# Optimization experiments

Measured on AMD Instinct MI355X. Metric: run time of the kernel, lower is better.

Reference implementation:

```python
import jax, jax.numpy as jnp
import numpy as np

N_P, N_V, N_C, N_A = 8000, 3000, 1500, 6000
CLS = N_C
D = 128
E = 150000
N_TOT = N_P + N_V + N_C + N_A
LAMBDA1 = 1.0


def _cal_matrix(A):
    # row-normalize, leaving all-zero rows untouched (matches cal_matrix)
    d = jnp.sum(A, axis=1)
    safe = jnp.where(d > 0, d, 1.0)
    return jnp.where((d > 0)[:, None], A / safe[:, None], A)


def _linear(x, W, b):
    return x @ W.T + b


def _gru(x, h, Wih, Whh, bih, bhh):
    # torch.nn.GRUCell semantics; gate order r, z, n
    gi = x @ Wih.T + bih
    gh = h @ Whh.T + bhh
    ir, iz, inn = jnp.split(gi, 3, axis=1)
    hr, hz, hn = jnp.split(gh, 3, axis=1)
    r = jax.nn.sigmoid(ir + hr)
    z = jax.nn.sigmoid(iz + hz)
    n = jnp.tanh(inn + r * hn)
    return (1.0 - z) * n + z * h


def _ce_soft(pred, label):
    # torch CrossEntropyLoss with probabilistic targets; NOTE: pred is already
    # softmaxed in the original, so log_softmax is applied on top (faithful double softmax)
    return -jnp.mean(jnp.sum(label * jax.nn.log_softmax(pred, axis=1), axis=1))


def _fuse(e0, e1, W2, b2, W3, b3):
    # attention fusion: leaky_relu(., 0) == relu; softmax over the NODE axis (faithful)
    a = jnp.concatenate([_linear(e0, W2, b2), _linear(e1, W3, b3)], axis=0)  # [2N,1]
    alpha = jax.nn.softmax(jax.nn.relu(a).reshape(2, -1, 1), axis=1)
    return jax.nn.relu(jnp.sum(alpha * jnp.stack([e0, e1], axis=0), axis=0))


def _forward(feat_P, feat_V, feat_C, feat_A, W1, b1, W2, b2, W3, b3,
             L00W, L00b, L01W, L01b, L10W, L10b, L11W, L11b, L12W, L12b,
             g0_Wih, g0_Whh, g0_bih, g0_bhh, g1_Wih, g1_Whh, g1_bih, g1_bhh,
             rel_emb, adj00, adj01, adj10, adj11, adj12, clsA, clsP, clsV, u_s, u_d):
    # self embeddings via shared linear1
    self_P = _linear(feat_P, W1, b1)
    self_V = _linear(feat_V, W1, b1)
    self_C = _linear(feat_C, W1, b1)
    self_A = _linear(feat_A, W1, b1)
    loss_tcp = jnp.float32(0.0)
    # ---- meta-path 0: V -> P -> A (GRUCell 0) ----
    pred = jax.nn.softmax(_linear(feat_V, L00W, L00b), axis=1)        # [N_V, CLS]
    loss_tcp += _ce_soft(pred, clsV)
    tcp = jnp.sum(pred * clsV, axis=1, keepdims=True)                 # bmm([N,1,C],[N,C,1])
    h = adj00 @ (tcp * feat_V)                                        # [N_P, D]
    state_P0 = _gru(feat_P, h, g0_Wih, g0_Whh, g0_bih, g0_bhh)
    pred = jax.nn.softmax(_linear(state_P0, L01W, L01b), axis=1)
    loss_tcp += _ce_soft(pred, clsP)
    tcp = jnp.sum(pred * clsP, axis=1, keepdims=True)
    h = adj01 @ (tcp * state_P0)                                      # [N_A, D]
    state_A0 = _gru(feat_A, h, g0_Wih, g0_Whh, g0_bih, g0_bhh)
    # ---- meta-path 1: A -> P -> V -> C (GRUCell 1) ----
    pred = jax.nn.softmax(_linear(feat_A, L10W, L10b), axis=1)
    loss_tcp += _ce_soft(pred, clsA)
    tcp = jnp.sum(pred * clsA, axis=1, keepdims=True)
    h = adj10 @ (tcp * feat_A)                                        # [N_P, D]
    state_P1 = _gru(feat_P, h, g1_Wih, g1_Whh, g1_bih, g1_bhh)        # appended 3rd, unused by fusion
    pred = jax.nn.softmax(_linear(state_P1, L11W, L11b), axis=1)
    loss_tcp += _ce_soft(pred, clsP)
    tcp = jnp.sum(pred * clsP, axis=1, keepdims=True)
    h = adj11 @ (tcp * state_P1)                                      # [N_V, D]
    state_V1 = _gru(feat_V, h, g1_Wih, g1_Whh, g1_bih, g1_bhh)
    pred = jax.nn.softmax(_linear(state_V1, L12W, L12b), axis=1)
    loss_tcp += _ce_soft(pred, clsV)
    tcp = jnp.sum(pred * clsV, axis=1, keepdims=True)
    h = adj12 @ (tcp * state_V1)                                      # [N_C, D]
    state_C1 = _gru(feat_C, h, g1_Wih, g1_Whh, g1_bih, g1_bhh)
    # ---- attention fusion of (self_emb, first GRU state) per node type ----
    emb_P = _fuse(self_P, state_P0, W2, b2, W3, b3)
    emb_V = _fuse(self_V, state_V1, W2, b2, W3, b3)
    emb_C = _fuse(self_C, state_C1, W2, b2, W3, b3)
    emb_A = _fuse(self_A, state_A0, W2, b2, W3, b3)
    final_ent = jnp.concatenate([emb_P, emb_V, emb_C, emb_A], axis=0)  # order P,V,C,A
    # ---- link scoring ----
    lab_d = u_d[:, 2].astype(jnp.float32)
    lab_s = u_s[:, 2].astype(jnp.float32)
    M_r = rel_emb[u_d[:, 3]]
    inner_d = jnp.sum(M_r * jnp.tanh(final_ent[u_d[:, 0]] + final_ent[u_d[:, 1]]), axis=1)
    inner_s = jnp.sum(final_ent[u_s[:, 0]] * final_ent[u_s[:, 1]], axis=1)
    base = -jnp.sum(jax.nn.log_sigmoid(lab_d * inner_d)) - jnp.sum(jax.nn.log_sigmoid(lab_s * inner_s))
    # l2_loss_emb is 0 in the original; l2_loss is computed but never added to loss_emb
    loss = base + LAMBDA1 * loss_tcp
    return loss, final_ent, rel_emb


def setup_inputs():
    key = jax.random.key(0)
    ki = iter(jax.random.split(key, 48))
    def nk():
        return next(ki)
    def xav(o, i):  # xavier_normal_
        return jax.random.normal(nk(), (o, i), jnp.float32) * jnp.sqrt(2.0 / (o + i))
    def uni(shape):  # torch GRUCell default init
        k = 1.0 / float(np.sqrt(D))
        return jax.random.uniform(nk(), shape, jnp.float32, -k, k)
    def radj(o, i, p=0.003):  # raw binary adjacency
        return (jax.random.uniform(nk(), (o, i)) < p).astype(jnp.float32)

    feat_P = jax.random.normal(nk(), (N_P, D), jnp.float32)
    feat_V = jax.random.normal(nk(), (N_V, D), jnp.float32)
    feat_C = jax.random.normal(nk(), (N_C, D), jnp.float32)
    feat_A = jax.random.normal(nk(), (N_A, D), jnp.float32)
    A00 = radj(N_P, N_V); A01 = radj(N_A, N_P)
    A10 = radj(N_P, N_A); A11 = radj(N_V, N_P); A12 = radj(N_C, N_V)

    inp = dict(
        feat_P=feat_P, feat_V=feat_V, feat_C=feat_C, feat_A=feat_A,
        W1=xav(D, D), b1=jnp.zeros((D,), jnp.float32),
        W2=xav(1, D), b2=jnp.zeros((1,), jnp.float32),
        W3=xav(1, D), b3=jnp.zeros((1,), jnp.float32),
        L00W=xav(CLS, D), L00b=jnp.zeros((CLS,), jnp.float32),
        L01W=xav(CLS, D), L01b=jnp.zeros((CLS,), jnp.float32),
        L10W=xav(CLS, D), L10b=jnp.zeros((CLS,), jnp.float32),
        L11W=xav(CLS, D), L11b=jnp.zeros((CLS,), jnp.float32),
        L12W=xav(CLS, D), L12b=jnp.zeros((CLS,), jnp.float32),
        g0_Wih=uni((3 * D, D)), g0_Whh=uni((3 * D, D)), g0_bih=uni((3 * D,)), g0_bhh=uni((3 * D,)),
        g1_Wih=uni((3 * D, D)), g1_Whh=uni((3 * D, D)), g1_bih=uni((3 * D,)), g1_bhh=uni((3 * D,)),
        rel_emb=jax.random.normal(nk(), (12, D), jnp.float32),
        adj00=_cal_matrix(A00), adj01=_cal_matrix(A01),
        adj10=_cal_matrix(A10), adj11=_cal_matrix(A11), adj12=_cal_matrix(A12),
        clsA=_cal_matrix((A12 @ (A11 @ A10)).T),   # [N_A, CLS]
        clsP=_cal_matrix((A12 @ A11).T),           # [N_P, CLS]
        clsV=_cal_matrix(A12.T),                   # [N_V, CLS]
    )

    def edges(n_cols):
        i = jax.random.randint(nk(), (E,), 0, N_TOT)
        j = jax.random.randint(nk(), (E,), 0, N_TOT)
        lab = jax.random.randint(nk(), (E,), 0, 2) * 2 - 1  # labels in {-1,+1}
        cols = [i, j, lab]
        if n_cols == 4:
            cols.append(jax.random.randint(nk(), (E,), 0, 12))
        return jnp.stack(cols, axis=1)

    inp['u_s'] = edges(3)
    inp['u_d'] = edges(4)
    return inp


def reference(feat_P, feat_V, feat_C, feat_A, W1, b1, W2, b2, W3, b3,
              L00W, L00b, L01W, L01b, L10W, L10b, L11W, L11b, L12W, L12b,
              g0_Wih, g0_Whh, g0_bih, g0_bhh, g1_Wih, g1_Whh, g1_bih, g1_bhh,
              rel_emb, adj00, adj01, adj10, adj11, adj12, clsA, clsP, clsV, u_s, u_d):
    return _forward(feat_P, feat_V, feat_C, feat_A, W1, b1, W2, b2, W3, b3,
                    L00W, L00b, L01W, L01b, L10W, L10b, L11W, L11b, L12W, L12b,
                    g0_Wih, g0_Whh, g0_bih, g0_bhh, g1_Wih, g1_Whh, g1_bih, g1_bhh,
                    rel_emb, adj00, adj01, adj10, adj11, adj12, clsA, clsP, clsV, u_s, u_d)
```

## Files before the change

### kernel.cpp

```cpp
#include <hip/hip_runtime.h>
#include <cstdint>
#include <cstddef>

#define DEV_INLINE __device__ __forceinline__

typedef __attribute__((ext_vector_type(8))) short bf16x8;
typedef __attribute__((ext_vector_type(16))) float f32x16;
struct __align__(8) US4 { unsigned short u[4]; };

DEV_INLINE unsigned short f2bf(float x) {
  unsigned u = __float_as_uint(x);
  return (unsigned short)((u + 0x7FFFu + ((u >> 16) & 1u)) >> 16);
}
DEV_INLINE float2 bfpair(unsigned v) {
  return make_float2(__uint_as_float(v << 16), __uint_as_float(v & 0xFFFF0000u));
}

struct CvtSeg { const float* src; unsigned short* dst; int n; int nblk; };
struct CvtArgs { CvtSeg seg[16]; int nseg; };

__global__ __launch_bounds__(256) void convert_bf16_many(CvtArgs args) {
  int b = blockIdx.x;
  int s = 0;
  while (s < args.nseg && b >= args.seg[s].nblk) { b -= args.seg[s].nblk; ++s; }
  if (s >= args.nseg) return;
  int base = b * 1024 + threadIdx.x * 4;
  if (base >= args.seg[s].n) return;
  float4 v = *reinterpret_cast<const float4*>(args.seg[s].src + base);
  US4 o;
  o.u[0] = f2bf(v.x); o.u[1] = f2bf(v.y); o.u[2] = f2bf(v.z); o.u[3] = f2bf(v.w);
  *reinterpret_cast<US4*>(args.seg[s].dst + base) = o;
}

DEV_INLINE void gemm_stage(const unsigned short* __restrict__ Xb,
                           const unsigned short* __restrict__ Wb,
                           int N, int O, int bm, int bn,
                           unsigned short* Xs, unsigned short* Ws)
{
  const int tid = threadIdx.x;
#pragma unroll
  for (int i = 0; i < 8; ++i) {
    int s = tid + 256 * i;
    int row = s >> 4, c16 = s & 15;
    uint4 v = make_uint4(0, 0, 0, 0);
    int gr = bm + row;
    if (gr < N) v = *reinterpret_cast<const uint4*>(Xb + (size_t)gr * 128 + c16 * 8);
    *reinterpret_cast<uint4*>(&Xs[(row * 16 + (c16 ^ (row & 7))) * 8]) = v;
  }
#pragma unroll
  for (int i = 0; i < 4; ++i) {
    int s = tid + 256 * i;
    int row = s >> 4, c16 = s & 15;
    uint4 v = make_uint4(0, 0, 0, 0);
    int gw = bn + row;
    if (gw < O) v = *reinterpret_cast<const uint4*>(Wb + (size_t)gw * 128 + c16 * 8);
    *reinterpret_cast<uint4*>(&Ws[(row * 16 + (c16 ^ (row & 7))) * 8]) = v;
  }
  __syncthreads();
}

DEV_INLINE void gemm_mfma(const unsigned short* Xs, const unsigned short* Ws,
                          f32x16& acc0, f32x16& acc1)
{
  const int tid = threadIdx.x;
  const int wave = tid >> 6, lane = tid & 63;
  const int l31 = lane & 31, lhi = lane >> 5;
#pragma unroll
  for (int i = 0; i < 16; ++i) { acc0[i] = 0.f; acc1[i] = 0.f; }
  const int ar = wave * 32 + l31;
#pragma unroll
  for (int ks = 0; ks < 8; ++ks) {
    int c16 = ks * 2 + lhi;
    bf16x8 a  = *reinterpret_cast<const bf16x8*>(&Xs[(ar * 16 + (c16 ^ (ar & 7))) * 8]);
    bf16x8 b0 = *reinterpret_cast<const bf16x8*>(&Ws[(l31 * 16 + (c16 ^ (l31 & 7))) * 8]);
    int br1 = 32 + l31;
    bf16x8 b1 = *reinterpret_cast<const bf16x8*>(&Ws[(br1 * 16 + (c16 ^ (br1 & 7))) * 8]);
    acc0 = __builtin_amdgcn_mfma_f32_32x32x16_bf16(a, b0, acc0, 0, 0, 0);
    acc1 = __builtin_amdgcn_mfma_f32_32x32x16_bf16(a, b1, acc1, 0, 0, 0);
  }
}

DEV_INLINE void gemm_body(
    const unsigned short* __restrict__ Xb, const unsigned short* __restrict__ Wb,
    const float* __restrict__ bias, float* __restrict__ C, int N, int O,
    int bm, int bn, unsigned short* Xs, unsigned short* Ws)
{
  gemm_stage(Xb, Wb, N, O, bm, bn, Xs, Ws);
  const int tid = threadIdx.x;
  const int wave = tid >> 6, lane = tid & 63;
  const int l31 = lane & 31, lhi = lane >> 5;
  f32x16 acc0, acc1;
  gemm_mfma(Xs, Ws, acc0, acc1);
#pragma unroll
  for (int reg = 0; reg < 16; ++reg) {
    int r = bm + wave * 32 + (reg & 3) + 8 * (reg >> 2) + 4 * lhi;
    if (r < N) {
      int c0 = bn + l31;
      if (c0 < O) C[(size_t)r * O + c0] = acc0[reg] + bias[c0];
      int c1 = bn + 32 + l31;
      if (c1 < O) C[(size_t)r * O + c1] = acc1[reg] + bias[c1];
    }
  }
}

DEV_INLINE void gemm_body_b(
    const unsigned short* __restrict__ Xb, const unsigned short* __restrict__ Wb,
    const float* __restrict__ bias, unsigned short* __restrict__ Cb, int N, int O,
    int bm, int bn, unsigned short* Xs, unsigned short* Ws)
{
  gemm_stage(Xb, Wb, N, O, bm, bn, Xs, Ws);
  const int tid = threadIdx.x;
  const int wave = tid >> 6, lane = tid & 63;
  const int l31 = lane & 31, lhi = lane >> 5;
  f32x16 acc0, acc1;
  gemm_mfma(Xs, Ws, acc0, acc1);
#pragma unroll
  for (int reg = 0; reg < 16; ++reg) {
    int r = bm + wave * 32 + (reg & 3) + 8 * (reg >> 2) + 4 * lhi;
    if (r < N) {
      int c0 = bn + l31;
      if (c0 < O) Cb[(size_t)r * O + c0] = f2bf(acc0[reg] + bias[c0]);
      int c1 = bn + 32 + l31;
      if (c1 < O) Cb[(size_t)r * O + c1] = f2bf(acc1[reg] + bias[c1]);
    }
  }
}

struct GSeg { const unsigned short* X; const unsigned short* W; const float* bias;
              float* C; int N; int O; int blk0; int xblk; };
struct GSegs { GSeg s[8]; int nseg; };

__global__ __launch_bounds__(256) void gemm_bf16_gseg(GSegs gs) {
  __shared__ __align__(16) unsigned short Xs[128 * 128];
  __shared__ __align__(16) unsigned short Ws[64 * 128];
  int bx = blockIdx.x;
  int si = 0;
  while (si + 1 < gs.nseg && bx >= gs.s[si + 1].blk0) ++si;
  const GSeg& g = gs.s[si];
  int b = bx - g.blk0;
  gemm_body(g.X, g.W, g.bias, g.C, g.N, g.O, (b % g.xblk) * 128, (b / g.xblk) * 64, Xs, Ws);
}

struct GBSeg { const unsigned short* X; const unsigned short* W; const float* bias;
               unsigned short* C; int N; int O; int blk0; int xblk; };
struct GBSegs { GBSeg s[4]; int nseg; };

__global__ __launch_bounds__(256) void gemm_bf16o_gseg(GBSegs gs) {
  __shared__ __align__(16) unsigned short Xs[128 * 128];
  __shared__ __align__(16) unsigned short Ws[64 * 128];
  int bx = blockIdx.x;
  int si = 0;
  while (si + 1 < gs.nseg && bx >= gs.s[si + 1].blk0) ++si;
  const GBSeg& g = gs.s[si];
  int b = bx - g.blk0;
  gemm_body_b(g.X, g.W, g.bias, g.C, g.N, g.O, (b % g.xblk) * 128, (b / g.xblk) * 64, Xs, Ws);
}

DEV_INLINE void spmv_body(const float* __restrict__ A, const float* __restrict__ Xs,
                          float* __restrict__ H, unsigned short* __restrict__ Hb,
                          int row, int K, float (*red)[128])
{
  int tid = threadIdx.x, wave = tid >> 6, lane = tid & 63;
  const float4* Arow = reinterpret_cast<const float4*>(A + (size_t)row * K);
  int K4 = K >> 2;
  float acc0 = 0.f, acc1 = 0.f;
  int base = wave * 64;
  int q = base + lane;
  float4 a = (base < K4 && q < K4) ? Arow[q] : make_float4(0.f, 0.f, 0.f, 0.f);
  for (; base < K4; base += 256) {
    int nb = base + 256;
    int nq = nb + lane;
    float4 an = (nb < K4 && nq < K4) ? Arow[nq] : make_float4(0.f, 0.f, 0.f, 0.f);
#pragma unroll
    for (int c = 0; c < 4; ++c) {
      float av = (c == 0) ? a.x : (c == 1) ? a.y : (c == 2) ? a.z : a.w;
      unsigned long long mm = __ballot(av != 0.f);
      while (mm) {
        int b = __builtin_ctzll(mm);
        mm &= mm - 1;
        float v = __shfl(av, b);
        int jj = (base + b) * 4 + c;
        const float* xr = Xs + (size_t)jj * 128;
        acc0 += v * xr[lane];
        acc1 += v * xr[lane + 64];
      }
    }
    a = an;
  }
  red[wave][lane] = acc0;
  red[wave][lane + 64] = acc1;
  __syncthreads();
  if (wave == 0) {
    float r0 = red[0][lane] + red[1][lane] + red[2][lane] + red[3][lane];
    float r1 = red[0][lane + 64] + red[1][lane + 64] + red[2][lane + 64] + red[3][lane + 64];
    H[(size_t)row * 128 + lane] = r0;
    H[(size_t)row * 128 + 64 + lane] = r1;
    Hb[(size_t)row * 128 + lane] = f2bf(r0);
    Hb[(size_t)row * 128 + 64 + lane] = f2bf(r1);
  }
}

__global__ __launch_bounds__(256) void spmv_scan(
    const float* __restrict__ A, const float* __restrict__ Xs,
    float* __restrict__ H, unsigned short* __restrict__ Hb, int M, int K)
{
  __shared__ float red[4][128];
  spmv_body(A, Xs, H, Hb, blockIdx.x, K, red);
}

__global__ __launch_bounds__(256) void spmv_scan2(
    const float* __restrict__ A0, const float* __restrict__ X0,
    float* __restrict__ H0, unsigned short* __restrict__ H0b, int M0, int K0,
    const float* __restrict__ A1, const float* __restrict__ X1,
    float* __restrict__ H1, unsigned short* __restrict__ H1b, int K1)
{
  __shared__ float red[4][128];
  if ((int)blockIdx.x < M0) spmv_body(A0, X0, H0, H0b, blockIdx.x, K0, red);
  else                      spmv_body(A1, X1, H1, H1b, blockIdx.x - M0, K1, red);
}

DEV_INLINE void ghgru_body(
    const unsigned short* __restrict__ Hb, const unsigned short* __restrict__ Whhb,
    const float* __restrict__ bhh, const float* __restrict__ gi,
    const float* __restrict__ hv, float* __restrict__ out,
    unsigned short* __restrict__ outb, int M, int bm, unsigned short* As)
{
  const int tid = threadIdx.x;
#pragma unroll
  for (int i = 0; i < 2; ++i) {
    int s = tid + 256 * i;
    int row = s >> 4, c16 = s & 15;
    uint4 v = make_uint4(0, 0, 0, 0);
    int gr = bm + row;
    if (gr < M) v = *reinterpret_cast<const uint4*>(Hb + (size_t)gr * 128 + c16 * 8);
    *reinterpret_cast<uint4*>(&As[(row * 16 + (c16 ^ (row & 7))) * 8]) = v;
  }
  __syncthreads();

  const int wave = tid >> 6, lane = tid & 63;
  const int l31 = lane & 31, lhi = lane >> 5;
  const int d = wave * 32 + l31;

  f32x16 ar, az, an;
#pragma unroll
  for (int i = 0; i < 16; ++i) { ar[i] = 0.f; az[i] = 0.f; an[i] = 0.f; }

#pragma unroll
  for (int ks = 0; ks < 8; ++ks) {
    int c16 = ks * 2 + lhi;
    bf16x8 a = *reinterpret_cast<const bf16x8*>(&As[(l31 * 16 + (c16 ^ (l31 & 7))) * 8]);
    const unsigned short* wb = Whhb + (size_t)c16 * 8;
    bf16x8 br = *reinterpret_cast<const bf16x8*>(wb + (size_t)d * 128);
    bf16x8 bz = *reinterpret_cast<const bf16x8*>(wb + (size_t)(128 + d) * 128);
    bf16x8 bn = *reinterpret_cast<const bf16x8*>(wb + (size_t)(256 + d) * 128);
    ar = __builtin_amdgcn_mfma_f32_32x32x16_bf16(a, br, ar, 0, 0, 0);
    az = __builtin_amdgcn_mfma_f32_32x32x16_bf16(a, bz, az, 0, 0, 0);
    an = __builtin_amdgcn_mfma_f32_32x32x16_bf16(a, bn, an, 0, 0, 0);
  }

  const float b_r = bhh[d], b_z = bhh[128 + d], b_n = bhh[256 + d];
#pragma unroll
  for (int reg = 0; reg < 16; ++reg) {
    int r = bm + (reg & 3) + 8 * (reg >> 2) + 4 * lhi;
    if (r < M) {
      const float* gir = gi + (size_t)r * 384;
      float rr = 1.f / (1.f + __expf(-(gir[d] + ar[reg] + b_r)));
      float zz = 1.f / (1.f + __expf(-(gir[128 + d] + az[reg] + b_z)));
      float nn = tanhf(gir[256 + d] + rr * (an[reg] + b_n));
      float h = hv[(size_t)r * 128 + d];
      float o = (1.f - zz) * nn + zz * h;
      out[(size_t)r * 128 + d] = o;
      outb[(size_t)r * 128 + d] = f2bf(o);
    }
  }
}

__global__ __launch_bounds__(256) void gh_gru(
    const unsigned short* __restrict__ Hb, const unsigned short* __restrict__ Whhb,
    const float* __restrict__ bhh, const float* __restrict__ gi,
    const float* __restrict__ hv, float* __restrict__ out,
    unsigned short* __restrict__ outb, int M)
{
  __shared__ __align__(16) unsigned short As[32 * 128];
  ghgru_body(Hb, Whhb, bhh, gi, hv, out, outb, M, blockIdx.x * 32, As);
}

__global__ __launch_bounds__(256) void gh_gru2(
    const unsigned short* Hb0, const unsigned short* Whh0, const float* bhh0,
    const float* gi0, const float* hv0, float* out0, unsigned short* outb0,
    int M0, int nblk0,
    const unsigned short* Hb1, const unsigned short* Whh1, const float* bhh1,
    const float* gi1, const float* hv1, float* out1, unsigned short* outb1, int M1)
{
  __shared__ __align__(16) unsigned short As[32 * 128];
  if ((int)blockIdx.x < nblk0)
    ghgru_body(Hb0, Whh0, bhh0, gi0, hv0, out0, outb0, M0, blockIdx.x * 32, As);
  else
    ghgru_body(Hb1, Whh1, bhh1, gi1, hv1, out1, outb1, M1, (blockIdx.x - nblk0) * 32, As);
}

DEV_INLINE void rowops_body(int lane, const float4* __restrict__ lr,
                            const float4* __restrict__ cr,
                            const float* __restrict__ srcrow,
                            float* __restrict__ scaledrow, float* __restrict__ cep)
{
  float4 e[6];
  float m = -3.4e38f;
#pragma unroll
  for (int k = 0; k < 6; ++k) {
    int idx = k * 64 + lane;
    if (idx < 375) {
      e[k] = lr[idx];
      m = fmaxf(m, fmaxf(fmaxf(e[k].x, e[k].y), fmaxf(e[k].z, e[k].w)));
    } else {
      e[k] = make_float4(-3.4e38f, -3.4e38f, -3.4e38f, -3.4e38f);
    }
  }
#pragma unroll
  for (int o = 1; o < 64; o <<= 1) m = fmaxf(m, __shfl_xor(m, o));
  float z = 0.f;
#pragma unroll
  for (int k = 0; k < 6; ++k) {
    e[k].x = __expf(e[k].x - m); e[k].y = __expf(e[k].y - m);
    e[k].z = __expf(e[k].z - m); e[k].w = __expf(e[k].w - m);
    z += (e[k].x + e[k].y) + (e[k].z + e[k].w);
  }
#pragma unroll
  for (int o = 1; o < 64; o <<= 1) z += __shfl_xor(z, o);
  float invZ1 = 1.0f / z;
  float m2 = invZ1;
  float t = 0.f, ls = 0.f, z2 = 0.f;
#pragma unroll
  for (int k = 0; k < 6; ++k) {
    int idx = k * 64 + lane;
    if (idx < 375) {
      float4 c = cr[idx];
      float px = e[k].x * invZ1, py = e[k].y * invZ1;
      float pz = e[k].z * invZ1, pw = e[k].w * invZ1;
      t  += c.x * px + c.y * py + c.z * pz + c.w * pw;
      ls += (c.x + c.y) + (c.z + c.w);
      z2 += __expf(px - m2) + __expf(py - m2) + __expf(pz - m2) + __expf(pw - m2);
    }
  }
#pragma unroll
  for (int o = 1; o < 64; o <<= 1) {
    t += __shfl_xor(t, o); ls += __shfl_xor(ls, o); z2 += __shfl_xor(z2, o);
  }
  if (lane == 0) *cep = t - ls * (m2 + logf(z2));
  scaledrow[lane]      = t * srcrow[lane];
  scaledrow[lane + 64] = t * srcrow[lane + 64];
}

__global__ __launch_bounds__(256) void rowops2(
    const float* lgA, const float* clsA_, const float* srcA, float* scA, float* ceA, int nA,
    const float* lgB, const float* clsB_, const float* srcB, float* scB, float* ceB, int nB)
{
  int gw = (blockIdx.x * 256 + threadIdx.x) >> 6;
  if (gw >= nA + nB) return;
  int lane = threadIdx.x & 63;
  if (gw < nA) {
    rowops_body(lane,
                reinterpret_cast<const float4*>(lgA + (size_t)gw * 1500),
                reinterpret_cast<const float4*>(clsA_ + (size_t)gw * 1500),
                srcA + (size_t)gw * 128, scA + (size_t)gw * 128, ceA + gw);
  } else {
    int r = gw - nA;
    rowops_body(lane,
                reinterpret_cast<const float4*>(lgB + (size_t)r * 1500),
                reinterpret_cast<const float4*>(clsB_ + (size_t)r * 1500),
                srcB + (size_t)r * 128, scB + (size_t)r * 128, ceB + r);
  }
}

DEV_INLINE void rowops_body_b(int lane, const unsigned* __restrict__ lrb,
                              const float2* __restrict__ cr2,
                              const float* __restrict__ srcrow,
                              float* __restrict__ scaledrow, float* __restrict__ cep)
{
  float2 e[12];
  float m = -3.4e38f;
#pragma unroll
  for (int k = 0; k < 12; ++k) {
    int idx = k * 64 + lane;
    if (idx < 750) {
      e[k] = bfpair(lrb[idx]);
      m = fmaxf(m, fmaxf(e[k].x, e[k].y));
    } else {
      e[k] = make_float2(-3.4e38f, -3.4e38f);
    }
  }
#pragma unroll
  for (int o = 1; o < 64; o <<= 1) m = fmaxf(m, __shfl_xor(m, o));
  float z = 0.f;
#pragma unroll
  for (int k = 0; k < 12; ++k) {
    e[k].x = __expf(e[k].x - m); e[k].y = __expf(e[k].y - m);
    z += e[k].x + e[k].y;
  }
#pragma unroll
  for (int o = 1; o < 64; o <<= 1) z += __shfl_xor(z, o);
  float invZ1 = 1.0f / z;
  float m2 = invZ1;
  float t = 0.f, ls = 0.f, z2 = 0.f;
#pragma unroll
  for (int k = 0; k < 12; ++k) {
    int idx = k * 64 + lane;
    if (idx < 750) {
      float2 c = cr2[idx];
      float px = e[k].x * invZ1, py = e[k].y * invZ1;
      t  += c.x * px + c.y * py;
      ls += c.x + c.y;
      z2 += __expf(px - m2) + __expf(py - m2);
    }
  }
#pragma unroll
  for (int o = 1; o < 64; o <<= 1) {
    t += __shfl_xor(t, o); ls += __shfl_xor(ls, o); z2 += __shfl_xor(z2, o);
  }
  if (lane == 0) *cep = t - ls * (m2 + logf(z2));
  scaledrow[lane]      = t * srcrow[lane];
  scaledrow[lane + 64] = t * srcrow[lane + 64];
}

__global__ __launch_bounds__(256) void rowops2b(
    const unsigned* lgA, const float* clsA_, const float* srcA, float* scA, float* ceA, int nA,
    const unsigned* lgB, const float* clsB_, const float* srcB, float* scB, float* ceB, int nB)
{
  int gw = (blockIdx.x * 256 + threadIdx.x) >> 6;
  if (gw >= nA + nB) return;
  int lane = threadIdx.x & 63;
  if (gw < nA) {
    rowops_body_b(lane, lgA + (size_t)gw * 750,
                  reinterpret_cast<const float2*>(clsA_ + (size_t)gw * 1500),
                  srcA + (size_t)gw * 128, scA + (size_t)gw * 128, ceA + gw);
  } else {
    int r = gw - nA;
    rowops_body_b(lane, lgB + (size_t)r * 750,
                  reinterpret_cast<const float2*>(clsB_ + (size_t)r * 1500),
                  srcB + (size_t)r * 128, scB + (size_t)r * 128, ceB + r);
  }
}

__global__ __launch_bounds__(256) void rowops1b(
    const unsigned* lg, const float* cls, const float* src, float* sc, float* ce, int n)
{
  int gw = (blockIdx.x * 256 + threadIdx.x) >> 6;
  if (gw >= n) return;
  int lane = threadIdx.x & 63;
  rowops_body_b(lane, lg + (size_t)gw * 750,
                reinterpret_cast<const float2*>(cls + (size_t)gw * 1500),
                src + (size_t)gw * 128, sc + (size_t)gw * 128, ce + gw);
}

__global__ __launch_bounds__(256) void fuse_scores_all(
    const float* __restrict__ e0, const float* __restrict__ e1,
    const float* __restrict__ W2, const float* __restrict__ b2,
    const float* __restrict__ W3, const float* __restrict__ b3,
    float* __restrict__ s0, float* __restrict__ s1)
{
  int lane = threadIdx.x & 63;
  int row = (blockIdx.x * 256 + threadIdx.x) >> 6;
  if (row >= 18500) return;
  float a0 = e0[(size_t)row * 128 + lane] * W2[lane] + e0[(size_t)row * 128 + 64 + lane] * W2[64 + lane];
  float a1 = e1[(size_t)row * 128 + lane] * W3[lane] + e1[(size_t)row * 128 + 64 + lane] * W3[64 + lane];
#pragma unroll
  for (int o = 32; o > 0; o >>= 1) { a0 += __shfl_down(a0, o); a1 += __shfl_down(a1, o); }
  if (lane == 0) {
    s0[row] = fmaxf(a0 + b2[0], 0.f);
    s1[row] = fmaxf(a1 + b3[0], 0.f);
  }
}

__global__ __launch_bounds__(1024) void denom4(
    const float* __restrict__ s0, const float* __restrict__ s1,
    float* __restrict__ den)
{
  __shared__ float red[1024];
  const int ns[4]   = {8000, 3000, 1500, 6000};
  const int offs[4] = {0, 8000, 11000, 12500};
  int b = blockIdx.x;
  int n = ns[b];
  const float* p0 = s0 + offs[b];
  const float* p1 = s1 + offs[b];
  int tid = threadIdx.x;
  float m = -3.4e38f;
  for (int i = tid; i < n; i += 1024) m = fmaxf(m, p0[i]);
  red[tid] = m; __syncthreads();
  for (int s = 512; s > 0; s >>= 1) { if (tid < s) red[tid] = fmaxf(red[tid], red[tid + s]); __syncthreads(); }
  float m0 = red[0]; __syncthreads();
  float z = 0.f;
  for (int i = tid; i < n; i += 1024) z += __expf(p0[i] - m0);
  red[tid] = z; __syncthreads();
  for (int s = 512; s > 0; s >>= 1) { if (tid < s) red[tid] += red[tid + s]; __syncthreads(); }
  float Z0 = red[0]; __syncthreads();
  m = -3.4e38f;
  for (int i = tid; i < n; i += 1024) m = fmaxf(m, p1[i]);
  red[tid] = m; __syncthreads();
  for (int s = 512; s > 0; s >>= 1) { if (tid < s) red[tid] = fmaxf(red[tid], red[tid + s]); __syncthreads(); }
  float m1 = red[0]; __syncthreads();
  z = 0.f;
  for (int i = tid; i < n; i += 1024) z += __expf(p1[i] - m1);
  red[tid] = z; __syncthreads();
  for (int s = 512; s > 0; s >>= 1) { if (tid < s) red[tid] += red[tid + s]; __syncthreads(); }
  if (tid == 0) { den[b * 4] = m0; den[b * 4 + 1] = Z0; den[b * 4 + 2] = m1; den[b * 4 + 3] = red[0]; }
}

__global__ __launch_bounds__(256) void fuse_emb_all(
    const float* __restrict__ e0, const float* __restrict__ e1,
    const float* __restrict__ s0, const float* __restrict__ s1,
    const float* __restrict__ den, const float* __restrict__ rel,
    float* __restrict__ fe, unsigned short* __restrict__ feb,
    float* __restrict__ rel_out, unsigned* __restrict__ ctr)
{
  int t = blockIdx.x * 256 + threadIdx.x;
  if (t == 0) *ctr = 0;
  const int tot2 = 18500 * 64;
  if (t < tot2) {
    int idx = t * 2;
    int row = idx >> 7;
    int e = (row < 8000) ? 0 : (row < 11000) ? 1 : (row < 12500) ? 2 : 3;
    float a0 = __expf(s0[row] - den[e * 4]) / den[e * 4 + 1];
    float a1 = __expf(s1[row] - den[e * 4 + 2]) / den[e * 4 + 3];
    float2 v0 = *reinterpret_cast<const float2*>(e0 + idx);
    float2 v1 = *reinterpret_cast<const float2*>(e1 + idx);
    float r0 = fmaxf(a0 * v0.x + a1 * v1.x, 0.f);
    float r1 = fmaxf(a0 * v0.y + a1 * v1.y, 0.f);
    *reinterpret_cast<float2*>(fe + idx) = make_float2(r0, r1);
    unsigned pb = (unsigned)f2bf(r0) | ((unsigned)f2bf(r1) << 16);
    *reinterpret_cast<unsigned*>(feb + idx) = pb;
  } else if (t < tot2 + 768) {
    int k = (t - tot2) * 2;
    *reinterpret_cast<float2*>(rel_out + k) = *reinterpret_cast<const float2*>(rel + k);
  }
}

__global__ __launch_bounds__(256) void edge_both_final(
    const int* __restrict__ ud, const int* __restrict__ us,
    const unsigned short* __restrict__ feb, const unsigned short* __restrict__ relb,
    float* __restrict__ partial, int En,
    const float* __restrict__ cebuf, unsigned* __restrict__ ctr,
    float* __restrict__ out)
{
  int lane = threadIdx.x & 63;
  int wid = threadIdx.x >> 6;
  bool is_d = (blockIdx.x < 1024);
  int bb = is_d ? blockIdx.x : blockIdx.x - 1024;
  int gw = bb * 4 + wid;
  const int nw = 1024 * 4;
  float acc = 0.f;
  if (is_d) {
    for (int e = gw; e < En; e += nw) {
      int4 ei = *reinterpret_cast<const int4*>(ud + (size_t)e * 4);
      float2 fi = bfpair(reinterpret_cast<const unsigned*>(feb + (size_t)ei.x * 128)[lane]);
      float2 fj = bfpair(reinterpret_cast<const unsigned*>(feb + (size_t)ei.y * 128)[lane]);
      float2 rr = bfpair(reinterpret_cast<const unsigned*>(relb + (size_t)ei.w * 128)[lane]);
      float d = rr.x * tanhf(fi.x + fj.x) + rr.y * tanhf(fi.y + fj.y);
#pragma unroll
      for (int o = 32; o > 0; o >>= 1) d += __shfl_down(d, o);
      if (lane == 0) {
        float x = (float)ei.z * d;
        acc += (x >= 0.f) ? log1pf(__expf(-x)) : (-x + log1pf(__expf(x)));
      }
    }
  } else {
    for (int e = gw; e < En; e += nw) {
      int i = us[(size_t)e * 3], j = us[(size_t)e * 3 + 1], lab = us[(size_t)e * 3 + 2];
      float2 fi = bfpair(reinterpret_cast<const unsigned*>(feb + (size_t)i * 128)[lane]);
      float2 fj = bfpair(reinterpret_cast<const unsigned*>(feb + (size_t)j * 128)[lane]);
      float d = fi.x * fj.x + fi.y * fj.y;
#pragma unroll
      for (int o = 32; o > 0; o >>= 1) d += __shfl_down(d, o);
      if (lane == 0) {
        float x = (float)lab * d;
        acc += (x >= 0.f) ? log1pf(__expf(-x)) : (-x + log1pf(__expf(x)));
      }
    }
  }
  __shared__ float red[4];
  if (lane == 0) red[wid] = acc;
  __syncthreads();
  __shared__ unsigned myturn;
  if (threadIdx.x == 0) {
    partial[blockIdx.x] = red[0] + red[1] + red[2] + red[3];
    __threadfence();
    myturn = atomicAdd(ctr, 1u);
  }
  __syncthreads();
  if (myturn == 2047) {
    __threadfence();
    __shared__ float red2[256];
    int tid = threadIdx.x;
    float a = 0.f;
    for (int i = tid; i < 2048; i += 256) a += partial[i];
    red2[tid] = a; __syncthreads();
    for (int s = 128; s > 0; s >>= 1) { if (tid < s) red2[tid] += red2[tid + s]; __syncthreads(); }
    float total = red2[0]; __syncthreads();
    const int ns[5] = {3000, 8000, 6000, 8000, 3000};
#pragma unroll
    for (int seg = 0; seg < 5; ++seg) {
      const float* v = cebuf + seg * 8000;
      float s = 0.f;
      for (int i = tid; i < ns[seg]; i += 256) s += v[i];
      red2[tid] = s; __syncthreads();
      for (int st = 128; st > 0; st >>= 1) { if (tid < st) red2[tid] += red2[tid + st]; __syncthreads(); }
      if (tid == 0) total -= red2[0] / (float)ns[seg];
      __syncthreads();
    }
    if (tid == 0) out[0] = total;
  }
}

extern "C" void kernel_launch(void* const* d_in, const int* in_sizes, int n_in,
                              void* d_out, int out_size, void* d_ws, size_t ws_size,
                              hipStream_t stream)
{
  const float* feat_P = (const float*)d_in[0];
  const float* feat_V = (const float*)d_in[1];
  const float* feat_C = (const float*)d_in[2];
  const float* feat_A = (const float*)d_in[3];
  const float* W1 = (const float*)d_in[4];
  const float* b1 = (const float*)d_in[5];
  const float* W2 = (const float*)d_in[6];
  const float* b2 = (const float*)d_in[7];
  const float* W3 = (const float*)d_in[8];
  const float* b3 = (const float*)d_in[9];
  const float* L00W = (const float*)d_in[10];
  const float* L00b = (const float*)d_in[11];
  const float* L01W = (const float*)d_in[12];
  const float* L01b = (const float*)d_in[13];
  const float* L10W = (const float*)d_in[14];
  const float* L10b = (const float*)d_in[15];
  const float* L11W = (const float*)d_in[16];
  const float* L11b = (const float*)d_in[17];
  const float* L12W = (const float*)d_in[18];
  const float* L12b = (const float*)d_in[19];
  const float* g0_Wih = (const float*)d_in[20];
  const float* g0_Whh = (const float*)d_in[21];
  const float* g0_bih = (const float*)d_in[22];
  const float* g0_bhh = (const float*)d_in[23];
  const float* g1_Wih = (const float*)d_in[24];
  const float* g1_Whh = (const float*)d_in[25];
  const float* g1_bih = (const float*)d_in[26];
  const float* g1_bhh = (const float*)d_in[27];
  const float* rel_emb = (const float*)d_in[28];
  const float* adj00 = (const float*)d_in[29];
  const float* adj01 = (const float*)d_in[30];
  const float* adj10 = (const float*)d_in[31];
  const float* adj11 = (const float*)d_in[32];
  const float* adj12 = (const float*)d_in[33];
  const float* clsA = (const float*)d_in[34];
  const float* clsP = (const float*)d_in[35];
  const float* clsV = (const float*)d_in[36];
  const int* u_s = (const int*)d_in[37];
  const int* u_d = (const int*)d_in[38];

  float* out = (float*)d_out;
  float* fe = out + 1;
  float* rel_out = out + 1 + 18500 * 128;

  float* ws = (float*)d_ws;
  size_t o = 0;
  auto alloc = [&](size_t n) { float* p = ws + o; o += n; return p; };
  float* selfb   = alloc((size_t)18500 * 128);
  float* stcat   = alloc((size_t)18500 * 128);
  float* stP1    = alloc((size_t)8000 * 128);
  float* gi      = alloc((size_t)26500 * 384);
  float* logits0 = alloc((size_t)3000 * 1500);
  float* logits2 = alloc((size_t)6000 * 1500);
  float* scaled0 = alloc((size_t)3000 * 128);
  float* scaled1 = alloc((size_t)8000 * 128);
  float* scaled2 = alloc((size_t)6000 * 128);
  float* scaled3 = alloc((size_t)8000 * 128);
  float* scaled4 = alloc((size_t)3000 * 128);
  float* h0      = alloc((size_t)8000 * 128);
  float* h2      = alloc((size_t)8000 * 128);
  float* h1      = alloc((size_t)6000 * 128);
  float* h3      = alloc((size_t)3000 * 128);
  float* h4      = alloc((size_t)1500 * 128);
  float* cebuf   = alloc(5 * 8000);
  float* s0b = alloc(18500);
  float* s1b = alloc(18500);
  float* den = alloc(16);
  float* partial = alloc(2048);
  unsigned* ctr = (unsigned*)alloc(4);
  auto allocb = [&](size_t nelem) { unsigned short* p = (unsigned short*)(ws + o); o += (nelem + 1) / 2; return p; };
  unsigned short* featb  = allocb((size_t)18500 * 128);
  unsigned short* stcatb = allocb((size_t)18500 * 128);
  unsigned short* stP1b  = allocb((size_t)8000 * 128);
  unsigned short* feb    = allocb((size_t)18500 * 128);
  unsigned short* h0b    = allocb((size_t)8000 * 128);
  unsigned short* h2b    = allocb((size_t)8000 * 128);
  unsigned short* h1b    = allocb((size_t)6000 * 128);
  unsigned short* h3b    = allocb((size_t)3000 * 128);
  unsigned short* h4b    = allocb((size_t)1500 * 128);
  unsigned short* lg1b   = allocb((size_t)8000 * 1500);
  unsigned short* lg3b   = allocb((size_t)8000 * 1500);
  unsigned short* relb   = allocb(12 * 128);
  unsigned short* W1b = allocb(128 * 128);
  unsigned short* L00Wb = allocb(1500 * 128);
  unsigned short* L01Wb = allocb(1500 * 128);
  unsigned short* L10Wb = allocb(1500 * 128);
  unsigned short* L11Wb = allocb(1500 * 128);
  unsigned short* L12Wb = allocb(1500 * 128);
  unsigned short* g0Wihb = allocb(384 * 128);
  unsigned short* g0Whhb = allocb(384 * 128);
  unsigned short* g1Wihb = allocb(384 * 128);
  unsigned short* g1Whhb = allocb(384 * 128);
  unsigned short* featPb = featb;
  unsigned short* featVb = featb + (size_t)8000 * 128;
  unsigned short* featCb = featb + (size_t)11000 * 128;
  unsigned short* featAb = featb + (size_t)12500 * 128;
  float* stP0 = stcat;
  float* stV1 = stcat + (size_t)8000 * 128;
  float* stC1 = stcat + (size_t)11000 * 128;
  float* stA0 = stcat + (size_t)12500 * 128;
  unsigned short* stP0b = stcatb;
  unsigned short* stV1b = stcatb + (size_t)8000 * 128;
  unsigned short* stC1b = stcatb + (size_t)11000 * 128;
  unsigned short* stA0b = stcatb + (size_t)12500 * 128;
  (void)ws_size; (void)in_sizes; (void)n_in; (void)out_size;

  dim3 blk(256);

  CvtArgs ca{};
  int nseg = 0, totblk = 0;
  auto addseg = [&](const float* src, unsigned short* dst, int n) {
    ca.seg[nseg].src = src; ca.seg[nseg].dst = dst; ca.seg[nseg].n = n;
    ca.seg[nseg].nblk = (n + 1023) / 1024; totblk += ca.seg[nseg].nblk; ++nseg;
  };
  addseg(feat_P, featPb, 8000 * 128);
  addseg(feat_V, featVb, 3000 * 128);
  addseg(feat_C, featCb, 1500 * 128);
  addseg(feat_A, featAb, 6000 * 128);
  addseg(W1, W1b, 128 * 128);
  addseg(L00W, L00Wb, 1500 * 128);
  addseg(L01W, L01Wb, 1500 * 128);
  addseg(L10W, L10Wb, 1500 * 128);
  addseg(L11W, L11Wb, 1500 * 128);
  addseg(L12W, L12Wb, 1500 * 128);
  addseg(g0_Wih, g0Wihb, 384 * 128);
  addseg(g0_Whh, g0Whhb, 384 * 128);
  addseg(g1_Wih, g1Wihb, 384 * 128);
  addseg(g1_Whh, g1Whhb, 384 * 128);
  addseg(rel_emb, relb, 12 * 128);
  ca.nseg = nseg;
  hipLaunchKernelGGL(convert_bf16_many, dim3(totblk), blk, 0, stream, ca);

  const size_t giOff[5] = {0, 8000, 14000, 22000, 25000};

  {
    GSegs gs{};
    int nb = 0, k = 0;
    auto add = [&](const unsigned short* X, const unsigned short* W, const float* bias,
                   float* C, int N, int O) {
      int xb = (N + 127) / 128, yb = (O + 63) / 64;
      gs.s[k] = GSeg{X, W, bias, C, N, O, nb, xb};
      nb += xb * yb; ++k;
    };
    add(featb,  W1b,    b1,     selfb,               18500, 128);
    add(featPb, g0Wihb, g0_bih, gi + giOff[0] * 384, 8000, 384);
    add(featAb, g0Wihb, g0_bih, gi + giOff[1] * 384, 6000, 384);
    add(featPb, g1Wihb, g1_bih, gi + giOff[2] * 384, 8000, 384);
    add(featVb, g1Wihb, g1_bih, gi + giOff[3] * 384, 3000, 384);
    add(featCb, g1Wihb, g1_bih, gi + giOff[4] * 384, 1500, 384);
    add(featVb, L00Wb,  L00b,   logits0,             3000, 1500);
    add(featAb, L10Wb,  L10b,   logits2,             6000, 1500);
    gs.nseg = k;
    hipLaunchKernelGGL(gemm_bf16_gseg, dim3(nb), blk, 0, stream, gs);
  }

  hipLaunchKernelGGL(rowops2, dim3((9000 * 64 + 255) / 256), blk, 0, stream,
                     logits0, clsV, feat_V, scaled0, cebuf + 0 * 8000, 3000,
                     logits2, clsA, feat_A, scaled2, cebuf + 2 * 8000, 6000);
  hipLaunchKernelGGL(spmv_scan2, dim3(16000), blk, 0, stream,
                     adj00, scaled0, h0, h0b, 8000, 3000,
                     adj10, scaled2, h2, h2b, 6000);
  hipLaunchKernelGGL(gh_gru2, dim3(500), blk, 0, stream,
                     h0b, g0Whhb, g0_bhh, gi + giOff[0] * 384, h0, stP0, stP0b, 8000, 250,
                     h2b, g1Whhb, g1_bhh, gi + giOff[2] * 384, h2, stP1, stP1b, 8000);
  {
    GBSegs gs{};
    gs.s[0] = GBSeg{stP0b, L01Wb, L01b, lg1b, 8000, 1500, 0,    63};
    gs.s[1] = GBSeg{stP1b, L11Wb, L11b, lg3b, 8000, 1500, 1512, 63};
    gs.nseg = 2;
    hipLaunchKernelGGL(gemm_bf16o_gseg, dim3(3024), blk, 0, stream, gs);
  }
  hipLaunchKernelGGL(rowops2b, dim3((16000 * 64 + 255) / 256), blk, 0, stream,
                     (const unsigned*)lg1b, clsP, stP0, scaled1, cebuf + 1 * 8000, 8000,
                     (const unsigned*)lg3b, clsP, stP1, scaled3, cebuf + 3 * 8000, 8000);
  hipLaunchKernelGGL(spmv_scan2, dim3(9000), blk, 0, stream,
                     adj01, scaled1, h1, h1b, 6000, 8000,
                     adj11, scaled3, h3, h3b, 8000);
  hipLaunchKernelGGL(gh_gru2, dim3(188 + 94), blk, 0, stream,
                     h1b, g0Whhb, g0_bhh, gi + giOff[1] * 384, h1, stA0, stA0b, 6000, 188,
                     h3b, g1Whhb, g1_bhh, gi + giOff[3] * 384, h3, stV1, stV1b, 3000);
  {
    GBSegs gs{};
    gs.s[0] = GBSeg{stV1b, L12Wb, L12b, lg1b, 3000, 1500, 0, 24};
    gs.nseg = 1;
    hipLaunchKernelGGL(gemm_bf16o_gseg, dim3(24 * 24), blk, 0, stream, gs);
  }
  hipLaunchKernelGGL(rowops1b, dim3((3000 * 64 + 255) / 256), blk, 0, stream,
                     (const unsigned*)lg1b, clsV, stV1, scaled4, cebuf + 4 * 8000, 3000);
  hipLaunchKernelGGL(spmv_scan, dim3(1500), blk, 0, stream, adj12, scaled4, h4, h4b, 1500, 3000);
  hipLaunchKernelGGL(gh_gru, dim3(47), blk, 0, stream,
                     h4b, g1Whhb, g1_bhh, gi + giOff[4] * 384, h4, stC1, stC1b, 1500);

  hipLaunchKernelGGL(fuse_scores_all, dim3((18500 + 3) / 4), blk, 0, stream,
                     selfb, stcat, W2, b2, W3, b3, s0b, s1b);
  hipLaunchKernelGGL(denom4, dim3(4), dim3(1024), 0, stream, s0b, s1b, den);
  hipLaunchKernelGGL(fuse_emb_all, dim3((18500 * 64 + 768 + 255) / 256), blk, 0, stream,
                     selfb, stcat, s0b, s1b, den, rel_emb, fe, feb, rel_out, ctr);

  hipLaunchKernelGGL(edge_both_final, dim3(2048), blk, 0, stream,
                     u_d, u_s, feb, relb, partial, 150000, cebuf, ctr, out);
}
```

Measured before the change: 603.2 us.

## Process two edges per wavefront with prefetch, fast tanh, separate final reduce

The edge-scoring kernel now splits each 64-lane wavefront into two half-waves, so each half handles one edge with 8-byte loads. The next edge's indices are prefetched, and tanhf is replaced by an exp-based approximation. The last-block atomic-counter reduction is replaced by a separate single-block final_reduce kernel. This aims to raise memory-level parallelism in the gather-heavy edge loop and cut transcendental cost, at the price of an extra kernel launch and slightly different tanh accuracy.

```diff
diff --git a/kernel.cpp b/kernel.cpp
--- a/kernel.cpp
+++ b/kernel.cpp
@@ -14,6 +14,13 @@
 }
 DEV_INLINE float2 bfpair(unsigned v) {
   return make_float2(__uint_as_float(v << 16), __uint_as_float(v & 0xFFFF0000u));
+}
+DEV_INLINE float ftanh(float x) {
+  float e = __expf(2.0f * x);
+  return 1.0f - 2.0f / (e + 1.0f);
+}
+DEV_INLINE float softplus_neg(float x) {
+  return (x >= 0.f) ? log1pf(__expf(-x)) : (-x + log1pf(__expf(x)));
 }
 
 struct CvtSeg { const float* src; unsigned short* dst; int n; int nblk; };
@@ -510,10 +517,9 @@
     const float* __restrict__ s0, const float* __restrict__ s1,
     const float* __restrict__ den, const float* __restrict__ rel,
     float* __restrict__ fe, unsigned short* __restrict__ feb,
-    float* __restrict__ rel_out, unsigned* __restrict__ ctr)
+    float* __restrict__ rel_out)
 {
   int t = blockIdx.x * 256 + threadIdx.x;
-  if (t == 0) *ctr = 0;
   const int tot2 = 18500 * 64;
   if (t < tot2) {
     int idx = t * 2;
@@ -534,80 +540,95 @@
   }
 }
 
-__global__ __launch_bounds__(256) void edge_both_final(
+__global__ __launch_bounds__(256) void edge_both(
     const int* __restrict__ ud, const int* __restrict__ us,
     const unsigned short* __restrict__ feb, const unsigned short* __restrict__ relb,
-    float* __restrict__ partial, int En,
-    const float* __restrict__ cebuf, unsigned* __restrict__ ctr,
-    float* __restrict__ out)
-{
-  int lane = threadIdx.x & 63;
-  int wid = threadIdx.x >> 6;
+    float* __restrict__ partial, int En)
+{
+  const int tid = threadIdx.x;
+  const int lane = tid & 63;
+  const int l = lane & 31, h = lane >> 5;
+  const int wid = tid >> 6;
   bool is_d = (blockIdx.x < 1024);
   int bb = is_d ? blockIdx.x : blockIdx.x - 1024;
-  int gw = bb * 4 + wid;
-  const int nw = 1024 * 4;
+  int e = (bb * 4 + wid) * 2 + h;
+  const int ns = 1024 * 4 * 2;
   float acc = 0.f;
   if (is_d) {
-    for (int e = gw; e < En; e += nw) {
-      int4 ei = *reinterpret_cast<const int4*>(ud + (size_t)e * 4);
-      float2 fi = bfpair(reinterpret_cast<const unsigned*>(feb + (size_t)ei.x * 128)[lane]);
-      float2 fj = bfpair(reinterpret_cast<const unsigned*>(feb + (size_t)ei.y * 128)[lane]);
-      float2 rr = bfpair(reinterpret_cast<const unsigned*>(relb + (size_t)ei.w * 128)[lane]);
-      float d = rr.x * tanhf(fi.x + fj.x) + rr.y * tanhf(fi.y + fj.y);
-#pragma unroll
-      for (int o = 32; o > 0; o >>= 1) d += __shfl_down(d, o);
-      if (lane == 0) {
-        float x = (float)ei.z * d;
-        acc += (x >= 0.f) ? log1pf(__expf(-x)) : (-x + log1pf(__expf(x)));
-      }
+    int4 ei = (e < En) ? *reinterpret_cast<const int4*>(ud + (size_t)e * 4)
+                       : make_int4(0, 0, 0, 0);
+    for (; e < En; e += ns) {
+      int en = e + ns;
+      int4 ein = (en < En) ? *reinterpret_cast<const int4*>(ud + (size_t)en * 4)
+                           : make_int4(0, 0, 0, 0);
+      uint2 a = reinterpret_cast<const uint2*>(feb + (size_t)ei.x * 128)[l];
+      uint2 b = reinterpret_cast<const uint2*>(feb + (size_t)ei.y * 128)[l];
+      uint2 r = reinterpret_cast<const uint2*>(relb + (size_t)ei.w * 128)[l];
+      float2 a0 = bfpair(a.x), a1 = bfpair(a.y);
+      float2 b0 = bfpair(b.x), b1 = bfpair(b.y);
+      float2 r0 = bfpair(r.x), r1 = bfpair(r.y);
+      float d = r0.x * ftanh(a0.x + b0.x) + r0.y * ftanh(a0.y + b0.y)
+              + r1.x * ftanh(a1.x + b1.x) + r1.y * ftanh(a1.y + b1.y);
+#pragma unroll
+      for (int o = 1; o < 32; o <<= 1) d += __shfl_xor(d, o);
+      if (l == 0) acc += softplus_neg((float)ei.z * d);
+      ei = ein;
     }
   } else {
-    for (int e = gw; e < En; e += nw) {
-      int i = us[(size_t)e * 3], j = us[(size_t)e * 3 + 1], lab = us[(size_t)e * 3 + 2];
-      float2 fi = bfpair(reinterpret_cast<const unsigned*>(feb + (size_t)i * 128)[lane]);
-      float2 fj = bfpair(reinterpret_cast<const unsigned*>(feb + (size_t)j * 128)[lane]);
-      float d = fi.x * fj.x + fi.y * fj.y;
-#pragma unroll
-      for (int o = 32; o > 0; o >>= 1) d += __shfl_down(d, o);
-      if (lane == 0) {
-        float x = (float)lab * d;
-        acc += (x >= 0.f) ? log1pf(__expf(-x)) : (-x + log1pf(__expf(x)));
-      }
-    }
-  }
-  __shared__ float red[4];
-  if (lane == 0) red[wid] = acc;
+    int3 ei = make_int3(0, 0, 0);
+    if (e < En) { ei.x = us[(size_t)e * 3]; ei.y = us[(size_t)e * 3 + 1]; ei.z = us[(size_t)e * 3 + 2]; }
+    for (; e < En; e += ns) {
+      int en = e + ns;
+      int3 ein = make_int3(0, 0, 0);
+      if (en < En) { ein.x = us[(size_t)en * 3]; ein.y = us[(size_t)en * 3 + 1]; ein.z = us[(size_t)en * 3 + 2]; }
+      uint2 a = reinterpret_cast<const uint2*>(feb + (size_t)ei.x * 128)[l];
+      uint2 b = reinterpret_cast<const uint2*>(feb + (size_t)ei.y * 128)[l];
+      float2 a0 = bfpair(a.x), a1 = bfpair(a.y);
+      float2 b0 = bfpair(b.x), b1 = bfpair(b.y);
+      float d = a0.x * b0.x + a0.y * b0.y + a1.x * b1.x + a1.y * b1.y;
+#pragma unroll
+      for (int o = 1; o < 32; o <<= 1) d += __shfl_xor(d, o);
+      if (l == 0) acc += softplus_neg((float)ei.z * d);
+      ei = ein;
+    }
+  }
+  __shared__ float red[8];
+  if (l == 0) red[wid * 2 + h] = acc;
   __syncthreads();
-  __shared__ unsigned myturn;
-  if (threadIdx.x == 0) {
-    partial[blockIdx.x] = red[0] + red[1] + red[2] + red[3];
-    __threadfence();
-    myturn = atomicAdd(ctr, 1u);
-  }
+  if (tid == 0) {
+    float s = 0.f;
+#pragma unroll
+    for (int i = 0; i < 8; ++i) s += red[i];
+    partial[blockIdx.x] = s;
+  }
+}
+
+__global__ __launch_bounds__(1024) void final_reduce(
+    const float* __restrict__ partial, const float* __restrict__ cebuf,
+    float* __restrict__ out)
+{
+  __shared__ float red[1024];
+  __shared__ float total;
+  int tid = threadIdx.x;
+  if (tid == 0) total = 0.f;
   __syncthreads();
-  if (myturn == 2047) {
-    __threadfence();
-    __shared__ float red2[256];
-    int tid = threadIdx.x;
-    float a = 0.f;
-    for (int i = tid; i < 2048; i += 256) a += partial[i];
-    red2[tid] = a; __syncthreads();
-    for (int s = 128; s > 0; s >>= 1) { if (tid < s) red2[tid] += red2[tid + s]; __syncthreads(); }
-    float total = red2[0]; __syncthreads();
-    const int ns[5] = {3000, 8000, 6000, 8000, 3000};
-#pragma unroll
-    for (int seg = 0; seg < 5; ++seg) {
-      const float* v = cebuf + seg * 8000;
-      float s = 0.f;
-      for (int i = tid; i < ns[seg]; i += 256) s += v[i];
-      red2[tid] = s; __syncthreads();
-      for (int st = 128; st > 0; st >>= 1) { if (tid < st) red2[tid] += red2[tid + st]; __syncthreads(); }
-      if (tid == 0) total -= red2[0] / (float)ns[seg];
-      __syncthreads();
-    }
-    if (tid == 0) out[0] = total;
-  }
+  float a = partial[tid] + partial[tid + 1024];
+  red[tid] = a; __syncthreads();
+  for (int s = 512; s > 0; s >>= 1) { if (tid < s) red[tid] += red[tid + s]; __syncthreads(); }
+  if (tid == 0) total += red[0];
+  __syncthreads();
+  const int ns[5] = {3000, 8000, 6000, 8000, 3000};
+#pragma unroll
+  for (int seg = 0; seg < 5; ++seg) {
+    const float* v = cebuf + seg * 8000;
+    float s = 0.f;
+    for (int i = tid; i < ns[seg]; i += 1024) s += v[i];
+    red[tid] = s; __syncthreads();
+    for (int st = 512; st > 0; st >>= 1) { if (tid < st) red[tid] += red[tid + st]; __syncthreads(); }
+    if (tid == 0) total -= red[0] / (float)ns[seg];
+    __syncthreads();
+  }
+  if (tid == 0) out[0] = total;
 }
 
 extern "C" void kernel_launch(void* const* d_in, const int* in_sizes, int n_in,
@@ -682,7 +703,6 @@
   float* s1b = alloc(18500);
   float* den = alloc(16);
   float* partial = alloc(2048);
-  unsigned* ctr = (unsigned*)alloc(4);
   auto allocb = [&](size_t nelem) { unsigned short* p = (unsigned short*)(ws + o); o += (nelem + 1) / 2; return p; };
   unsigned short* featb  = allocb((size_t)18500 * 128);
   unsigned short* stcatb = allocb((size_t)18500 * 128);
@@ -810,8 +830,9 @@
                      selfb, stcat, W2, b2, W3, b3, s0b, s1b);
   hipLaunchKernelGGL(denom4, dim3(4), dim3(1024), 0, stream, s0b, s1b, den);
   hipLaunchKernelGGL(fuse_emb_all, dim3((18500 * 64 + 768 + 255) / 256), blk, 0, stream,
-                     selfb, stcat, s0b, s1b, den, rel_emb, fe, feb, rel_out, ctr);
-
-  hipLaunchKernelGGL(edge_both_final, dim3(2048), blk, 0, stream,
-                     u_d, u_s, feb, relb, partial, 150000, cebuf, ctr, out);
-}
+                     selfb, stcat, s0b, s1b, den, rel_emb, fe, feb, rel_out);
+
+  hipLaunchKernelGGL(edge_both, dim3(2048), blk, 0, stream, u_d, u_s, feb, relb, partial, 150000);
+
+  hipLaunchKernelGGL(final_reduce, dim3(1), dim3(1024), 0, stream, partial, cebuf, out);
+}
```

After: 516.0 us. 1.17x faster.
